# Performance work log

Measured on AMD Instinct MI355X. Metric: run time of the kernel, lower is better.

The kernel has to match this reference:

```python
import jax, jax.numpy as jnp
import numpy as np

N, E, B = 200000, 800000, 16
NODE_FEAT = 140  # last col = shape element type id
N_OPS, N_TYPES = 120, 8
OP_EMB, TYPE_EMB, CFG = 32, 4, 18
H = 64
CAT = (NODE_FEAT - 1) + TYPE_EMB + OP_EMB + CFG  # 193


def _lin(k, i, o):
    s = 1.0 / np.sqrt(i)
    return jax.random.uniform(k, (i, o), jnp.float32, -s, s)


def setup_inputs() -> dict:
    key = jax.random.key(0)
    ks = jax.random.split(key, 20)
    nf = jax.random.normal(ks[0], (N, NODE_FEAT - 1), jnp.float32)
    ty = jax.random.randint(ks[1], (N, 1), 0, N_TYPES).astype(jnp.float32)
    inp = {
        "node_feat": jnp.concatenate([nf, ty], axis=1),
        "node_config_feat": jax.random.normal(ks[2], (N, CFG), jnp.float32),
        "node_opcode": jax.random.randint(ks[3], (N,), 0, N_OPS),
        "edge_index": jax.random.randint(ks[4], (2, E), 0, N),
        "batch": jnp.sort(jax.random.randint(ks[5], (N,), 0, B)),
        "op_emb": jax.random.normal(ks[6], (N_OPS, OP_EMB), jnp.float32),
        "type_emb": jax.random.normal(ks[7], (N_TYPES, TYPE_EMB), jnp.float32),
        "lin_w": _lin(ks[8], CAT, 2 * H),
        "lin_b": jnp.zeros((2 * H,), jnp.float32),
        "post_w": _lin(ks[9], H, 1),
        "post_b": jnp.zeros((1,), jnp.float32),
    }
    kk = 10
    for l, ind in enumerate([2 * H, H, H]):
        inp[f"p{l}_wp"] = _lin(ks[kk], ind, ind); kk += 1  # SAGE project lin
        inp[f"p{l}_bp"] = jnp.zeros((ind,), jnp.float32)
        inp[f"p{l}_wl"] = _lin(ks[kk], ind, H); kk += 1    # lin_l (on aggregated)
        inp[f"p{l}_bl"] = jnp.zeros((H,), jnp.float32)
        inp[f"p{l}_wr"] = _lin(ks[kk], ind, H); kk += 1    # lin_r (root, no bias)
    return inp


def _sage(x, src, dst, deg_inv, wp, bp, wl, bl, wr):
    # PyG SAGEConv(project=True, normalize=True), mean aggregation
    xp = jax.nn.relu(x @ wp + bp)
    agg = jax.ops.segment_sum(xp[src], dst, num_segments=x.shape[0]) * deg_inv
    out = agg @ wl + bl + x @ wr
    n = jnp.linalg.norm(out, axis=-1, keepdims=True)
    return out / jnp.maximum(n, 1e-12)


def reference(node_feat, node_config_feat, node_opcode, edge_index, batch,
              op_emb, type_emb, lin_w, lin_b, post_w, post_b,
              p0_wp, p0_bp, p0_wl, p0_bl, p0_wr,
              p1_wp, p1_bp, p1_wl, p1_bl, p1_wr,
              p2_wp, p2_bp, p2_wl, p2_bl, p2_wr):
    lps = [(p0_wp, p0_bp, p0_wl, p0_bl, p0_wr),
           (p1_wp, p1_bp, p1_wl, p1_bl, p1_wr),
           (p2_wp, p2_bp, p2_wl, p2_bl, p2_wr)]
    ty = jnp.take(type_emb, node_feat[:, -1].astype(jnp.int32), axis=0)
    op = jnp.take(op_emb, node_opcode, axis=0)
    x = jnp.concatenate([node_feat[:, :-1], ty, op, node_config_feat], axis=-1)
    x = jax.nn.relu(x @ lin_w + lin_b)  # (N, 128)
    src, dst = edge_index[0], edge_index[1]
    deg = jax.ops.segment_sum(jnp.ones((E,), x.dtype), dst, num_segments=N)
    deg_inv = (1.0 / jnp.maximum(deg, 1.0))[:, None]
    for (wp, bp, wl, bl, wr) in lps:
        x = _sage(x, src, dst, deg_inv, wp, bp, wl, bl, wr)
    # global max + mean pool per graph
    gmax = jax.ops.segment_max(x, batch, num_segments=B)
    gsum = jax.ops.segment_sum(x, batch, num_segments=B)
    cnt = jax.ops.segment_sum(jnp.ones((N,), x.dtype), batch, num_segments=B)
    g = gmax + gsum / jnp.maximum(cnt, 1.0)[:, None]
    g = g / jnp.linalg.norm(g, axis=-1, keepdims=True)
    return g @ post_w + post_b  # (B, 1); eval path returns x_graph
```

## Files before the change

kernel.cpp:

```cpp
#include <hip/hip_runtime.h>

typedef _Float16 half8 __attribute__((ext_vector_type(8)));
typedef _Float16 h4 __attribute__((ext_vector_type(4)));
typedef _Float16 h2 __attribute__((ext_vector_type(2)));
typedef float f32x4 __attribute__((ext_vector_type(4)));

__device__ __forceinline__ unsigned fkey(float f) {
  unsigned u = __float_as_uint(f);
  return (u & 0x80000000u) ? ~u : (u | 0x80000000u);
}
__device__ __forceinline__ float funkey(unsigned k) {
  unsigned u = (k & 0x80000000u) ? (k ^ 0x80000000u) : ~k;
  return __uint_as_float(u);
}

struct WD { const float* src; _Float16* dst; int K, NC, Kpad, base; };
struct WDs { WD d[10]; int total; };

__global__ __launch_bounds__(256) void k_wconv(WDs w) {
  int idx = blockIdx.x * 256 + threadIdx.x;
  if (idx >= w.total) return;
#pragma unroll
  for (int i = 0; i < 10; ++i) {
    int rel = idx - w.d[i].base;
    int sz = w.d[i].NC * w.d[i].Kpad;
    if (rel >= 0 && rel < sz) {
      int n = rel / w.d[i].Kpad;
      int k = rel - n * w.d[i].Kpad;
      w.d[i].dst[rel] = (k < w.d[i].K) ? (_Float16)w.d[i].src[(size_t)k * w.d[i].NC + n]
                                       : (_Float16)0.f;
      return;
    }
  }
}

__global__ __launch_bounds__(256) void k_count(const int* __restrict__ dst,
                                               int* __restrict__ counts, int E) {
  int e = blockIdx.x * 256 + threadIdx.x;
  if (e < E) atomicAdd(&counts[dst[e]], 1);
}

__global__ __launch_bounds__(256) void k_scan1(const int* __restrict__ counts,
                                               int* __restrict__ offsets,
                                               int* __restrict__ blockSums, int N) {
  __shared__ int sm[256];
  int tid = threadIdx.x;
  int gid = blockIdx.x * 256 + tid;
  int v = (gid < N) ? counts[gid] : 0;
  sm[tid] = v;
  __syncthreads();
  for (int off = 1; off < 256; off <<= 1) {
    int t = (tid >= off) ? sm[tid - off] : 0;
    __syncthreads();
    sm[tid] += t;
    __syncthreads();
  }
  if (gid < N) offsets[gid] = sm[tid] - v;
  if (tid == 255) blockSums[blockIdx.x] = sm[255];
}

__global__ __launch_bounds__(1024) void k_scan2(int* __restrict__ blockSums, int NB) {
  __shared__ int sm[1024];
  int tid = threadIdx.x;
  int v = (tid < NB) ? blockSums[tid] : 0;
  sm[tid] = v;
  __syncthreads();
  for (int off = 1; off < 1024; off <<= 1) {
    int t = (tid >= off) ? sm[tid - off] : 0;
    __syncthreads();
    sm[tid] += t;
    __syncthreads();
  }
  if (tid < NB) blockSums[tid] = sm[tid] - v;
}

__global__ __launch_bounds__(256) void k_scan3(const int* __restrict__ counts,
                                               int* __restrict__ offsets,
                                               const int* __restrict__ blockSums,
                                               int* __restrict__ fillpos,
                                               float* __restrict__ deginv, int N, int E) {
  int gid = blockIdx.x * 256 + threadIdx.x;
  if (gid < N) {
    int off = offsets[gid] + blockSums[gid >> 8];
    offsets[gid] = off;
    fillpos[gid] = off;
    deginv[gid] = 1.f / fmaxf((float)counts[gid], 1.f);
  }
  if (gid == 0) offsets[N] = E;
}

__global__ __launch_bounds__(256) void k_fill(const int* __restrict__ src,
                                              const int* __restrict__ dst,
                                              int* __restrict__ fillpos,
                                              int* __restrict__ esrc, int E) {
  int e = blockIdx.x * 256 + threadIdx.x;
  if (e < E) {
    int p = atomicAdd(&fillpos[dst[e]], 1);
    esrc[p] = src[e];
  }
}

__device__ __forceinline__ half8 build_feat8(int r, int c0,
    const float* __restrict__ node_feat, const float* __restrict__ cfgf,
    const int* __restrict__ opcode, const float* __restrict__ op_emb,
    const float* __restrict__ type_emb) {
  const float* fr = node_feat + (size_t)r * 140;
  float v[8];
  if (c0 <= 128) {
    float4 a = *(const float4*)(fr + c0);
    float4 b = *(const float4*)(fr + c0 + 4);
    v[0] = a.x; v[1] = a.y; v[2] = a.z; v[3] = a.w;
    v[4] = b.x; v[5] = b.y; v[6] = b.z; v[7] = b.w;
  } else if (c0 == 136) {
    v[0] = fr[136]; v[1] = fr[137]; v[2] = fr[138];
    int ty = min(max((int)fr[139], 0), 7);
    const float* te = type_emb + ty * 4;
    v[3] = te[0]; v[4] = te[1]; v[5] = te[2]; v[6] = te[3];
    v[7] = op_emb[opcode[r] * 32 + 0];
  } else if (c0 < 168) {
    const float* o = op_emb + opcode[r] * 32 + (c0 - 143);
#pragma unroll
    for (int j = 0; j < 8; ++j) v[j] = o[j];
  } else if (c0 == 168) {
    const float* o = op_emb + opcode[r] * 32;
#pragma unroll
    for (int j = 0; j < 7; ++j) v[j] = o[25 + j];
    v[7] = cfgf[(size_t)r * 18 + 0];
  } else if (c0 < 192) {
    const float* c = cfgf + (size_t)r * 18 + (c0 - 175);
#pragma unroll
    for (int j = 0; j < 8; ++j) v[j] = c[j];
  } else if (c0 == 192) {
    v[0] = cfgf[(size_t)r * 18 + 17];
#pragma unroll
    for (int j = 1; j < 8; ++j) v[j] = 0.f;
  } else {
#pragma unroll
    for (int j = 0; j < 8; ++j) v[j] = 0.f;
  }
  half8 o;
#pragma unroll
  for (int j = 0; j < 8; ++j) o[j] = (_Float16)v[j];
  return o;
}

__global__ __launch_bounds__(256) void k_mmF(
    const float* __restrict__ node_feat, const float* __restrict__ cfgf,
    const int* __restrict__ opcode, const float* __restrict__ op_emb,
    const float* __restrict__ type_emb,
    const _Float16* __restrict__ W0, const float* __restrict__ bias,
    _Float16* __restrict__ Out, int N) {
  constexpr int K0 = 224, NC = 128;
  constexpr int NT = NC / 16;

  const int lane = threadIdx.x & 63, wave = threadIdx.x >> 6;
  const int quad = lane >> 4, l15 = lane & 15;
  const int r0 = blockIdx.x * 64 + wave * 16;

  f32x4 acc[NT];
#pragma unroll
  for (int t = 0; t < NT; ++t) acc[t] = (f32x4)0.f;

#pragma unroll
  for (int k = 0; k < K0; k += 32) {
    int r = min(r0 + l15, N - 1);
    half8 a = build_feat8(r, quad * 8 + k, node_feat, cfgf, opcode, op_emb, type_emb);
#pragma unroll
    for (int t = 0; t < NT; ++t) {
      half8 b = *(const half8*)(W0 + (size_t)(t * 16 + l15) * K0 + quad * 8 + k);
      acc[t] = __builtin_amdgcn_mfma_f32_16x16x32_f16(a, b, acc[t], 0, 0, 0);
    }
  }

#pragma unroll
  for (int t = 0; t < NT; ++t) {
    float bv = bias[t * 16 + l15];
    acc[t][0] = fmaxf(acc[t][0] + bv, 0.f);
    acc[t][1] = fmaxf(acc[t][1] + bv, 0.f);
    acc[t][2] = fmaxf(acc[t][2] + bv, 0.f);
    acc[t][3] = fmaxf(acc[t][3] + bv, 0.f);
  }
#pragma unroll
  for (int j = 0; j < 4; ++j) {
    int r = r0 + quad * 4 + j;
    if (r < N) {
#pragma unroll
      for (int t = 0; t < NT; ++t)
        Out[(size_t)r * NC + t * 16 + l15] = (_Float16)acc[t][j];
    }
  }
}

template <int K0, int K1, int NC, int MODE>
__global__ __launch_bounds__(256) void k_mm(
    const _Float16* __restrict__ A0, const _Float16* __restrict__ W0,
    const _Float16* __restrict__ A1, const _Float16* __restrict__ W1,
    const float* __restrict__ bias, _Float16* __restrict__ Out, int N) {
  constexpr int NT = NC / 16;
  constexpr int RT = 4;
  constexpr int KP0 = K0 + 8;
  constexpr int KP1 = K1 + 8;
  __shared__ _Float16 sB0[NC * KP0];
  __shared__ _Float16 sB1[(K1 > 0) ? (NC * KP1) : 8];

  for (int idx = threadIdx.x; idx < NC * (K0 / 8); idx += 256) {
    int nn = idx / (K0 / 8), k8 = idx - nn * (K0 / 8);
    *(half8*)(sB0 + nn * KP0 + k8 * 8) = *(const half8*)(W0 + (size_t)nn * K0 + k8 * 8);
  }
  if constexpr (K1 > 0) {
    for (int idx = threadIdx.x; idx < NC * (K1 / 8); idx += 256) {
      int nn = idx / (K1 / 8), k8 = idx - nn * (K1 / 8);
      *(half8*)(sB1 + nn * KP1 + k8 * 8) = *(const half8*)(W1 + (size_t)nn * K1 + k8 * 8);
    }
  }
  __syncthreads();

  const int lane = threadIdx.x & 63, wave = threadIdx.x >> 6;
  const int quad = lane >> 4, l15 = lane & 15;
  const int r0 = blockIdx.x * 256 + wave * 64;

  f32x4 acc[RT][NT];
#pragma unroll
  for (int rt = 0; rt < RT; ++rt)
#pragma unroll
    for (int t = 0; t < NT; ++t) acc[rt][t] = (f32x4)0.f;

  {
    const _Float16* ap = A0 + (size_t)(r0 + l15) * K0 + quad * 8;
#pragma unroll
    for (int k = 0; k < K0; k += 32) {
      half8 a[RT];
#pragma unroll
      for (int rt = 0; rt < RT; ++rt) a[rt] = *(const half8*)(ap + (size_t)rt * 16 * K0 + k);
#pragma unroll
      for (int t = 0; t < NT; ++t) {
        half8 b = *(const half8*)(sB0 + (t * 16 + l15) * KP0 + quad * 8 + k);
#pragma unroll
        for (int rt = 0; rt < RT; ++rt)
          acc[rt][t] = __builtin_amdgcn_mfma_f32_16x16x32_f16(a[rt], b, acc[rt][t], 0, 0, 0);
      }
    }
  }
  if constexpr (K1 > 0) {
    const _Float16* ap = A1 + (size_t)(r0 + l15) * K1 + quad * 8;
#pragma unroll
    for (int k = 0; k < K1; k += 32) {
      half8 a[RT];
#pragma unroll
      for (int rt = 0; rt < RT; ++rt) a[rt] = *(const half8*)(ap + (size_t)rt * 16 * K1 + k);
#pragma unroll
      for (int t = 0; t < NT; ++t) {
        half8 b = *(const half8*)(sB1 + (t * 16 + l15) * KP1 + quad * 8 + k);
#pragma unroll
        for (int rt = 0; rt < RT; ++rt)
          acc[rt][t] = __builtin_amdgcn_mfma_f32_16x16x32_f16(a[rt], b, acc[rt][t], 0, 0, 0);
      }
    }
  }

#pragma unroll
  for (int rt = 0; rt < RT; ++rt) {
#pragma unroll
    for (int t = 0; t < NT; ++t) {
      float bv = bias[t * 16 + l15];
      acc[rt][t][0] += bv; acc[rt][t][1] += bv;
      acc[rt][t][2] += bv; acc[rt][t][3] += bv;
    }
    if constexpr (MODE == 1) {
      f32x4 ss = (f32x4)0.f;
#pragma unroll
      for (int t = 0; t < NT; ++t) ss += acc[rt][t] * acc[rt][t];
#pragma unroll
      for (int j = 0; j < 4; ++j) {
        float s = ss[j];
        s += __shfl_xor(s, 1);
        s += __shfl_xor(s, 2);
        s += __shfl_xor(s, 4);
        s += __shfl_xor(s, 8);
        float sc = 1.f / fmaxf(sqrtf(s), 1e-12f);
#pragma unroll
        for (int t = 0; t < NT; ++t) acc[rt][t][j] *= sc;
      }
    } else {
#pragma unroll
      for (int t = 0; t < NT; ++t) {
        acc[rt][t][0] = fmaxf(acc[rt][t][0], 0.f);
        acc[rt][t][1] = fmaxf(acc[rt][t][1], 0.f);
        acc[rt][t][2] = fmaxf(acc[rt][t][2], 0.f);
        acc[rt][t][3] = fmaxf(acc[rt][t][3], 0.f);
      }
    }
#pragma unroll
    for (int j = 0; j < 4; ++j) {
      int r = r0 + rt * 16 + quad * 4 + j;
      if (r < N) {
#pragma unroll
        for (int t = 0; t < NT; ++t)
          Out[(size_t)r * NC + t * 16 + l15] = (_Float16)acc[rt][t][j];
      }
    }
  }
}

template <int NC>
__global__ __launch_bounds__(256) void k_agg(const _Float16* __restrict__ xp,
                                             const int* __restrict__ offs,
                                             const int* __restrict__ esrc,
                                             const float* __restrict__ deginv,
                                             _Float16* __restrict__ agg, int N) {
  constexpr int LPN = NC / 4;
  int t = blockIdx.x * 256 + threadIdx.x;
  int node = t / LPN;
  int lane = t - node * LPN;
  if (node >= N) return;
  int s0 = offs[node], s1 = offs[node + 1];
  float a0 = 0.f, a1 = 0.f, a2 = 0.f, a3 = 0.f;
  for (int i = s0; i < s1; i += 4) {
    int nlast = s1 - 1;
    int e0 = esrc[i];
    int e1 = esrc[min(i + 1, nlast)];
    int e2 = esrc[min(i + 2, nlast)];
    int e3 = esrc[min(i + 3, nlast)];
    h4 v0 = ((const h4*)(xp + (size_t)e0 * NC))[lane];
    h4 v1 = ((const h4*)(xp + (size_t)e1 * NC))[lane];
    h4 v2 = ((const h4*)(xp + (size_t)e2 * NC))[lane];
    h4 v3 = ((const h4*)(xp + (size_t)e3 * NC))[lane];
    a0 += (float)v0[0]; a1 += (float)v0[1]; a2 += (float)v0[2]; a3 += (float)v0[3];
    if (i + 1 < s1) { a0 += (float)v1[0]; a1 += (float)v1[1]; a2 += (float)v1[2]; a3 += (float)v1[3]; }
    if (i + 2 < s1) { a0 += (float)v2[0]; a1 += (float)v2[1]; a2 += (float)v2[2]; a3 += (float)v2[3]; }
    if (i + 3 < s1) { a0 += (float)v3[0]; a1 += (float)v3[1]; a2 += (float)v3[2]; a3 += (float)v3[3]; }
  }
  float di = deginv[node];
  h4 o;
  o[0] = (_Float16)(a0 * di); o[1] = (_Float16)(a1 * di);
  o[2] = (_Float16)(a2 * di); o[3] = (_Float16)(a3 * di);
  ((h4*)(agg + (size_t)node * NC))[lane] = o;
}

__global__ __launch_bounds__(256) void k_pool1(const _Float16* __restrict__ x,
                                               const int* __restrict__ batch,
                                               unsigned* __restrict__ gkey,
                                               float* __restrict__ gsum,
                                               int* __restrict__ gcnt, int N) {
  int chunk = blockIdx.x * 4 + (threadIdx.x >> 6);
  int lane = threadIdx.x & 63;
  int n0 = chunk * 64;
  if (n0 >= N) return;
  int n1 = min(n0 + 64, N);
  float rmax = -3.4e38f, rsum = 0.f;
  int rcnt = 0, curb = batch[n0];
  for (int n = n0; n < n1; ++n) {
    int b = batch[n];
    if (b != curb) {
      atomicMax(&gkey[curb * 64 + lane], fkey(rmax));
      atomicAdd(&gsum[curb * 64 + lane], rsum);
      if (lane == 0) atomicAdd(&gcnt[curb], rcnt);
      rmax = -3.4e38f; rsum = 0.f; rcnt = 0; curb = b;
    }
    float v = (float)x[(size_t)n * 64 + lane];
    rmax = fmaxf(rmax, v);
    rsum += v;
    rcnt++;
  }
  atomicMax(&gkey[curb * 64 + lane], fkey(rmax));
  atomicAdd(&gsum[curb * 64 + lane], rsum);
  if (lane == 0) atomicAdd(&gcnt[curb], rcnt);
}

__global__ __launch_bounds__(1024) void k_pool2(const unsigned* __restrict__ gkey,
                                                const float* __restrict__ gsum,
                                                const int* __restrict__ gcnt,
                                                const float* __restrict__ post_w,
                                                const float* __restrict__ post_b,
                                                float* __restrict__ out) {
  int b = threadIdx.x >> 6, lane = threadIdx.x & 63;
  float m = funkey(gkey[b * 64 + lane]);
  float s = gsum[b * 64 + lane];
  float c = (float)gcnt[b];
  float g = m + s / fmaxf(c, 1.f);
  float ss = g * g;
#pragma unroll
  for (int off = 1; off < 64; off <<= 1) ss += __shfl_xor(ss, off);
  float gn = g / fmaxf(sqrtf(ss), 1e-30f);
  float contrib = gn * post_w[lane];
#pragma unroll
  for (int off = 1; off < 64; off <<= 1) contrib += __shfl_xor(contrib, off);
  if (lane == 0) out[b] = contrib + post_b[0];
}

extern "C" void kernel_launch(void* const* d_in, const int* in_sizes, int n_in,
                              void* d_out, int out_size, void* d_ws, size_t ws_size,
                              hipStream_t stream) {
  const float* node_feat = (const float*)d_in[0];
  const float* cfgf      = (const float*)d_in[1];
  const int*   opcode    = (const int*)d_in[2];
  const int*   eidx      = (const int*)d_in[3];
  const int*   batch     = (const int*)d_in[4];
  const float* op_emb    = (const float*)d_in[5];
  const float* type_emb  = (const float*)d_in[6];
  const float* lin_w     = (const float*)d_in[7];
  const float* lin_b     = (const float*)d_in[8];
  const float* post_w    = (const float*)d_in[9];
  const float* post_b    = (const float*)d_in[10];
  const float* wp[3] = {(const float*)d_in[11], (const float*)d_in[16], (const float*)d_in[21]};
  const float* bp[3] = {(const float*)d_in[12], (const float*)d_in[17], (const float*)d_in[22]};
  const float* wl[3] = {(const float*)d_in[13], (const float*)d_in[18], (const float*)d_in[23]};
  const float* bl[3] = {(const float*)d_in[14], (const float*)d_in[19], (const float*)d_in[24]};
  const float* wr[3] = {(const float*)d_in[15], (const float*)d_in[20], (const float*)d_in[25]};

  const int N = in_sizes[2];
  const int E = in_sizes[3] / 2;
  const int NPAD = ((N + 255) / 256) * 256;
  const int* e_src = eidx;
  const int* e_dst = eidx + E;

  char* p = (char*)d_ws;
  auto alloc = [&](size_t bytes) -> void* {
    void* r = (void*)p;
    p += (bytes + 255) & ~(size_t)255;
    return r;
  };
  _Float16* X1 = (_Float16*)alloc((size_t)NPAD * 128 * 2);
  _Float16* R2 = (_Float16*)alloc((size_t)NPAD * 128 * 2);
  _Float16* R3 = (_Float16*)alloc((size_t)NPAD * 128 * 2);
  _Float16* WT = (_Float16*)alloc(86016 * 2);
  int* counts    = (int*)alloc((size_t)N * 4);
  int* offsets   = (int*)alloc((size_t)(N + 1) * 4);
  int* fillpos   = (int*)alloc((size_t)N * 4);
  float* deginv  = (float*)alloc((size_t)N * 4);
  int* blockSums = (int*)alloc(1024 * 4);
  int* esrc      = (int*)alloc((size_t)E * 4);
  unsigned* gkey = (unsigned*)alloc(16 * 64 * 4);
  float* gsum    = (float*)alloc(16 * 64 * 4);
  int* gcnt      = (int*)alloc(16 * 4);
  (void)ws_size; (void)n_in; (void)out_size;

  _Float16* WTenc = WT + 0;
  _Float16* WTp0  = WT + 28672;
  _Float16* WTl0  = WT + 45056;
  _Float16* WTr0  = WT + 53248;
  _Float16* WTp1  = WT + 61440;
  _Float16* WTl1  = WT + 65536;
  _Float16* WTr1  = WT + 69632;
  _Float16* WTp2  = WT + 73728;
  _Float16* WTl2  = WT + 77824;
  _Float16* WTr2  = WT + 81920;

  WDs wds;
  wds.d[0] = {lin_w, WTenc, 193, 128, 224, 0};
  wds.d[1] = {wp[0], WTp0, 128, 128, 128, 28672};
  wds.d[2] = {wl[0], WTl0, 128, 64, 128, 45056};
  wds.d[3] = {wr[0], WTr0, 128, 64, 128, 53248};
  wds.d[4] = {wp[1], WTp1, 64, 64, 64, 61440};
  wds.d[5] = {wl[1], WTl1, 64, 64, 64, 65536};
  wds.d[6] = {wr[1], WTr1, 64, 64, 64, 69632};
  wds.d[7] = {wp[2], WTp2, 64, 64, 64, 73728};
  wds.d[8] = {wl[2], WTl2, 64, 64, 64, 77824};
  wds.d[9] = {wr[2], WTr2, 64, 64, 64, 81920};
  wds.total = 86016;

  hipMemsetAsync(counts, 0, (size_t)N * 4, stream);
  hipMemsetAsync(gkey, 0, 16 * 64 * 4, stream);
  hipMemsetAsync(gsum, 0, 16 * 64 * 4, stream);
  hipMemsetAsync(gcnt, 0, 16 * 4, stream);
  if (NPAD > N) {
    const size_t tail = (size_t)(NPAD - N) * 128 * 2;
    hipMemsetAsync(X1 + (size_t)N * 128, 0, tail, stream);
    hipMemsetAsync(R2 + (size_t)N * 128, 0, tail, stream);
    hipMemsetAsync(R3 + (size_t)N * 128, 0, tail, stream);
  }

  const int nbE = (E + 255) / 256;
  const int nbN = (N + 255) / 256;
  const int nbMM = NPAD / 256;
  const int nbMMF = NPAD / 64;
  const int nbA128 = ((size_t)N * 32 + 255) / 256;
  const int nbA64  = ((size_t)N * 16 + 255) / 256;
  const int nbP = ((N + 63) / 64 + 3) / 4;

  k_wconv<<<(86016 + 255) / 256, 256, 0, stream>>>(wds);
  k_count<<<nbE, 256, 0, stream>>>(e_dst, counts, E);
  k_scan1<<<nbN, 256, 0, stream>>>(counts, offsets, blockSums, N);
  k_scan2<<<1, 1024, 0, stream>>>(blockSums, nbN);
  k_scan3<<<nbN, 256, 0, stream>>>(counts, offsets, blockSums, fillpos, deginv, N, E);
  k_fill<<<nbE, 256, 0, stream>>>(e_src, e_dst, fillpos, esrc, E);

  k_mmF<<<nbMMF, 256, 0, stream>>>(node_feat, cfgf, opcode, op_emb, type_emb,
                                   WTenc, lin_b, X1, N);

  k_mm<128, 0, 128, 0><<<nbMM, 256, 0, stream>>>(X1, WTp0, nullptr, nullptr, bp[0], R2, N);
  k_agg<128><<<nbA128, 256, 0, stream>>>(R2, offsets, esrc, deginv, R3, N);
  k_mm<128, 128, 64, 1><<<nbMM, 256, 0, stream>>>(R3, WTl0, X1, WTr0, bl[0], R2, N);
  k_mm<64, 0, 64, 0><<<nbMM, 256, 0, stream>>>(R2, WTp1, nullptr, nullptr, bp[1], R3, N);
  k_agg<64><<<nbA64, 256, 0, stream>>>(R3, offsets, esrc, deginv, X1, N);
  k_mm<64, 64, 64, 1><<<nbMM, 256, 0, stream>>>(X1, WTl1, R2, WTr1, bl[1], R3, N);
  k_mm<64, 0, 64, 0><<<nbMM, 256, 0, stream>>>(R3, WTp2, nullptr, nullptr, bp[2], X1, N);
  k_agg<64><<<nbA64, 256, 0, stream>>>(X1, offsets, esrc, deginv, R2, N);
  k_mm<64, 64, 64, 1><<<nbMM, 256, 0, stream>>>(R2, WTl2, R3, WTr2, bl[2], X1, N);

  k_pool1<<<nbP, 256, 0, stream>>>(X1, batch, gkey, gsum, gcnt, N);
  k_pool2<<<1, 1024, 0, stream>>>(gkey, gsum, gcnt, post_w, post_b, (float*)d_out);
}
```

Baseline: 692.9 us.

## Precompute opcode and type embedding projections into lookup tables for encoder matmul

The encoder's op and type embedding columns are folded algebraically into small precomputed tables: op_emb@W and type_emb@W plus bias. Each row then adds table lookups to its accumulator instead of gathering embeddings into the matmul input. This cuts the encoder GEMM K dimension from 224 to 160 and removes the branchy per-element feature build. It adds two small setup kernels and keeps the table terms in fp32 rather than fp16, which slightly changes numerics.

Result: no change. 688.7 us (-0.6%).

```diff
diff --git a/kernel.cpp b/kernel.cpp
--- a/kernel.cpp
+++ b/kernel.cpp
@@ -12,6 +12,13 @@
 __device__ __forceinline__ float funkey(unsigned k) {
   unsigned u = (k & 0x80000000u) ? (k ^ 0x80000000u) : ~k;
   return __uint_as_float(u);
+}
+
+__device__ __forceinline__ half8 cvt8(float4 a, float4 b) {
+  half8 o;
+  o[0] = (_Float16)a.x; o[1] = (_Float16)a.y; o[2] = (_Float16)a.z; o[3] = (_Float16)a.w;
+  o[4] = (_Float16)b.x; o[5] = (_Float16)b.y; o[6] = (_Float16)b.z; o[7] = (_Float16)b.w;
+  return o;
 }
 
 struct WD { const float* src; _Float16* dst; int K, NC, Kpad, base; };
@@ -31,6 +38,39 @@
                                        : (_Float16)0.f;
       return;
     }
+  }
+}
+
+__global__ __launch_bounds__(256) void k_wenc2(const float* __restrict__ lin_w,
+                                               _Float16* __restrict__ dst) {
+  int idx = blockIdx.x * 256 + threadIdx.x;
+  if (idx >= 128 * 160) return;
+  int n = idx / 160, k = idx - n * 160;
+  float v = (k < 139) ? lin_w[(size_t)k * 128 + n]
+                      : ((k < 157) ? lin_w[(size_t)(k + 36) * 128 + n] : 0.f);
+  dst[idx] = (_Float16)v;
+}
+
+__global__ __launch_bounds__(256) void k_tab(const float* __restrict__ lin_w,
+                                             const float* __restrict__ lin_b,
+                                             const float* __restrict__ op_emb,
+                                             const float* __restrict__ type_emb,
+                                             float* __restrict__ OPT,
+                                             float* __restrict__ TYTb) {
+  int idx = blockIdx.x * 256 + threadIdx.x;
+  if (idx < 120 * 128) {
+    int o = idx >> 7, n = idx & 127;
+    float s = 0.f;
+#pragma unroll
+    for (int k = 0; k < 32; ++k) s += op_emb[o * 32 + k] * lin_w[(size_t)(143 + k) * 128 + n];
+    OPT[idx] = s;
+  } else if (idx < 120 * 128 + 8 * 128) {
+    int rel = idx - 120 * 128;
+    int t = rel >> 7, n = rel & 127;
+    float s = lin_b[n];
+#pragma unroll
+    for (int k = 0; k < 4; ++k) s += type_emb[t * 4 + k] * lin_w[(size_t)(139 + k) * 128 + n];
+    TYTb[rel] = s;
   }
 }
 
@@ -100,93 +140,90 @@
   }
 }
 
-__device__ __forceinline__ half8 build_feat8(int r, int c0,
-    const float* __restrict__ node_feat, const float* __restrict__ cfgf,
-    const int* __restrict__ opcode, const float* __restrict__ op_emb,
-    const float* __restrict__ type_emb) {
-  const float* fr = node_feat + (size_t)r * 140;
-  float v[8];
-  if (c0 <= 128) {
-    float4 a = *(const float4*)(fr + c0);
-    float4 b = *(const float4*)(fr + c0 + 4);
-    v[0] = a.x; v[1] = a.y; v[2] = a.z; v[3] = a.w;
-    v[4] = b.x; v[5] = b.y; v[6] = b.z; v[7] = b.w;
-  } else if (c0 == 136) {
-    v[0] = fr[136]; v[1] = fr[137]; v[2] = fr[138];
-    int ty = min(max((int)fr[139], 0), 7);
-    const float* te = type_emb + ty * 4;
-    v[3] = te[0]; v[4] = te[1]; v[5] = te[2]; v[6] = te[3];
-    v[7] = op_emb[opcode[r] * 32 + 0];
-  } else if (c0 < 168) {
-    const float* o = op_emb + opcode[r] * 32 + (c0 - 143);
-#pragma unroll
-    for (int j = 0; j < 8; ++j) v[j] = o[j];
-  } else if (c0 == 168) {
-    const float* o = op_emb + opcode[r] * 32;
-#pragma unroll
-    for (int j = 0; j < 7; ++j) v[j] = o[25 + j];
-    v[7] = cfgf[(size_t)r * 18 + 0];
-  } else if (c0 < 192) {
-    const float* c = cfgf + (size_t)r * 18 + (c0 - 175);
-#pragma unroll
-    for (int j = 0; j < 8; ++j) v[j] = c[j];
-  } else if (c0 == 192) {
-    v[0] = cfgf[(size_t)r * 18 + 17];
-#pragma unroll
-    for (int j = 1; j < 8; ++j) v[j] = 0.f;
-  } else {
-#pragma unroll
-    for (int j = 0; j < 8; ++j) v[j] = 0.f;
-  }
-  half8 o;
-#pragma unroll
-  for (int j = 0; j < 8; ++j) o[j] = (_Float16)v[j];
-  return o;
-}
-
 __global__ __launch_bounds__(256) void k_mmF(
     const float* __restrict__ node_feat, const float* __restrict__ cfgf,
-    const int* __restrict__ opcode, const float* __restrict__ op_emb,
-    const float* __restrict__ type_emb,
-    const _Float16* __restrict__ W0, const float* __restrict__ bias,
-    _Float16* __restrict__ Out, int N) {
-  constexpr int K0 = 224, NC = 128;
-  constexpr int NT = NC / 16;
+    const int* __restrict__ opcode,
+    const float* __restrict__ OPT, const float* __restrict__ TYTb,
+    const _Float16* __restrict__ W0, _Float16* __restrict__ Out, int N) {
+  constexpr int NC = 128, NT = NC / 16, KP = 160;
 
   const int lane = threadIdx.x & 63, wave = threadIdx.x >> 6;
   const int quad = lane >> 4, l15 = lane & 15;
   const int r0 = blockIdx.x * 64 + wave * 16;
 
+  int opc[4], ty[4];
+#pragma unroll
+  for (int j = 0; j < 4; ++j) {
+    int rw = min(r0 + quad * 4 + j, N - 1);
+    opc[j] = opcode[rw];
+    ty[j] = min(max((int)node_feat[(size_t)rw * 140 + 139], 0), 7);
+  }
   f32x4 acc[NT];
 #pragma unroll
-  for (int t = 0; t < NT; ++t) acc[t] = (f32x4)0.f;
-
-#pragma unroll
-  for (int k = 0; k < K0; k += 32) {
-    int r = min(r0 + l15, N - 1);
-    half8 a = build_feat8(r, quad * 8 + k, node_feat, cfgf, opcode, op_emb, type_emb);
+  for (int t = 0; t < NT; ++t) {
+#pragma unroll
+    for (int j = 0; j < 4; ++j)
+      acc[t][j] = OPT[opc[j] * 128 + t * 16 + l15] + TYTb[ty[j] * 128 + t * 16 + l15];
+  }
+
+  const int rA = min(r0 + l15, N - 1);
+  const float* fr = node_feat + (size_t)rA * 140;
+  const float* cg = cfgf + (size_t)rA * 18;
+  half8 A[5];
+#pragma unroll
+  for (int k = 0; k < 4; ++k) {
+    float4 a = *(const float4*)(fr + quad * 8 + k * 32);
+    float4 b = *(const float4*)(fr + quad * 8 + k * 32 + 4);
+    A[k] = cvt8(a, b);
+  }
+  if (quad == 0) {
+    A[4] = cvt8(*(const float4*)(fr + 128), *(const float4*)(fr + 132));
+  } else if (quad == 1) {
+    float4 a = *(const float4*)(fr + 136);
+    float2 c0 = *(const float2*)(cg + 0), c1 = *(const float2*)(cg + 2),
+           c2 = *(const float2*)(cg + 4);
+    A[4][0] = (_Float16)a.x;  A[4][1] = (_Float16)a.y;  A[4][2] = (_Float16)a.z;
+    A[4][3] = (_Float16)c0.x; A[4][4] = (_Float16)c0.y; A[4][5] = (_Float16)c1.x;
+    A[4][6] = (_Float16)c1.y; A[4][7] = (_Float16)c2.x;
+  } else if (quad == 2) {
+    float2 c0 = *(const float2*)(cg + 4), c1 = *(const float2*)(cg + 6),
+           c2 = *(const float2*)(cg + 8), c3 = *(const float2*)(cg + 10),
+           c4 = *(const float2*)(cg + 12);
+    A[4][0] = (_Float16)c0.y; A[4][1] = (_Float16)c1.x; A[4][2] = (_Float16)c1.y;
+    A[4][3] = (_Float16)c2.x; A[4][4] = (_Float16)c2.y; A[4][5] = (_Float16)c3.x;
+    A[4][6] = (_Float16)c3.y; A[4][7] = (_Float16)c4.x;
+  } else {
+    float2 c0 = *(const float2*)(cg + 12), c1 = *(const float2*)(cg + 14),
+           c2 = *(const float2*)(cg + 16);
+    A[4][0] = (_Float16)c0.y; A[4][1] = (_Float16)c1.x; A[4][2] = (_Float16)c1.y;
+    A[4][3] = (_Float16)c2.x; A[4][4] = (_Float16)c2.y;
+    A[4][5] = (_Float16)0.f;  A[4][6] = (_Float16)0.f;  A[4][7] = (_Float16)0.f;
+  }
+
+  const _Float16* Wb = W0 + (size_t)l15 * KP + quad * 8;
+#pragma unroll
+  for (int k = 0; k < 5; ++k) {
 #pragma unroll
     for (int t = 0; t < NT; ++t) {
-      half8 b = *(const half8*)(W0 + (size_t)(t * 16 + l15) * K0 + quad * 8 + k);
-      acc[t] = __builtin_amdgcn_mfma_f32_16x16x32_f16(a, b, acc[t], 0, 0, 0);
+      half8 b = *(const half8*)(Wb + (size_t)t * 16 * KP + k * 32);
+      acc[t] = __builtin_amdgcn_mfma_f32_16x16x32_f16(A[k], b, acc[t], 0, 0, 0);
     }
   }
 
 #pragma unroll
   for (int t = 0; t < NT; ++t) {
-    float bv = bias[t * 16 + l15];
-    acc[t][0] = fmaxf(acc[t][0] + bv, 0.f);
-    acc[t][1] = fmaxf(acc[t][1] + bv, 0.f);
-    acc[t][2] = fmaxf(acc[t][2] + bv, 0.f);
-    acc[t][3] = fmaxf(acc[t][3] + bv, 0.f);
+    acc[t][0] = fmaxf(acc[t][0], 0.f);
+    acc[t][1] = fmaxf(acc[t][1], 0.f);
+    acc[t][2] = fmaxf(acc[t][2], 0.f);
+    acc[t][3] = fmaxf(acc[t][3], 0.f);
   }
 #pragma unroll
   for (int j = 0; j < 4; ++j) {
-    int r = r0 + quad * 4 + j;
-    if (r < N) {
+    int rw = r0 + quad * 4 + j;
+    if (rw < N) {
 #pragma unroll
       for (int t = 0; t < NT; ++t)
-        Out[(size_t)r * NC + t * 16 + l15] = (_Float16)acc[t][j];
+        Out[(size_t)rw * NC + t * 16 + l15] = (_Float16)acc[t][j];
     }
   }
 }
@@ -433,6 +470,8 @@
   unsigned* gkey = (unsigned*)alloc(16 * 64 * 4);
   float* gsum    = (float*)alloc(16 * 64 * 4);
   int* gcnt      = (int*)alloc(16 * 4);
+  float* OPT     = (float*)alloc(120 * 128 * 4);
+  float* TYTb    = (float*)alloc(8 * 128 * 4);
   (void)ws_size; (void)n_in; (void)out_size;
 
   _Float16* WTenc = WT + 0;
@@ -447,7 +486,7 @@
   _Float16* WTr2  = WT + 81920;
 
   WDs wds;
-  wds.d[0] = {lin_w, WTenc, 193, 128, 224, 0};
+  wds.d[0] = {lin_w, WTenc, 0, 0, 1, 0};
   wds.d[1] = {wp[0], WTp0, 128, 128, 128, 28672};
   wds.d[2] = {wl[0], WTl0, 128, 64, 128, 45056};
   wds.d[3] = {wr[0], WTr0, 128, 64, 128, 53248};
@@ -479,14 +518,16 @@
   const int nbP = ((N + 63) / 64 + 3) / 4;
 
   k_wconv<<<(86016 + 255) / 256, 256, 0, stream>>>(wds);
+  k_wenc2<<<(128 * 160 + 255) / 256, 256, 0, stream>>>(lin_w, WTenc);
+  k_tab<<<(120 * 128 + 8 * 128 + 255) / 256, 256, 0, stream>>>(lin_w, lin_b, op_emb,
+                                                               type_emb, OPT, TYTb);
   k_count<<<nbE, 256, 0, stream>>>(e_dst, counts, E);
   k_scan1<<<nbN, 256, 0, stream>>>(counts, offsets, blockSums, N);
   k_scan2<<<1, 1024, 0, stream>>>(blockSums, nbN);
   k_scan3<<<nbN, 256, 0, stream>>>(counts, offsets, blockSums, fillpos, deginv, N, E);
   k_fill<<<nbE, 256, 0, stream>>>(e_src, e_dst, fillpos, esrc, E);
 
-  k_mmF<<<nbMMF, 256, 0, stream>>>(node_feat, cfgf, opcode, op_emb, type_emb,
-                                   WTenc, lin_b, X1, N);
+  k_mmF<<<nbMMF, 256, 0, stream>>>(node_feat, cfgf, opcode, OPT, TYTb, WTenc, X1, N);
 
   k_mm<128, 0, 128, 0><<<nbMM, 256, 0, stream>>>(X1, WTp0, nullptr, nullptr, bp[0], R2, N);
   k_agg<128><<<nbA128, 256, 0, stream>>>(R2, offsets, esrc, deginv, R3, N);
```
